# Kernel tuning notes

Hardware: AMD Instinct MI355X
Metric: run time of the kernel (lower is better)

## Reference

```python
import jax, jax.numpy as jnp
import numpy as np

E = 4      # num_ensemble
DIN = 256  # input_dim
D = 256    # d_model (output_dim)
B = 16
T = 1024
LN_EPS = 1e-5


def setup_inputs() -> dict:
    key = jax.random.key(0)
    ks = jax.random.split(key, 14)
    s = 0.02
    x = jax.random.normal(ks[0], (B, T, DIN), dtype=jnp.float32)
    in_proj_w = s * jax.random.normal(ks[1], (3, E, DIN, D), dtype=jnp.float32)
    in_proj_b = jnp.zeros((3, E, D), dtype=jnp.float32)
    mid_w = s * jax.random.normal(ks[2], (2, E, D, D), dtype=jnp.float32)
    mid_b = jnp.zeros((2, E, D), dtype=jnp.float32)
    ff_w1 = s * jax.random.normal(ks[3], (E, D, D), dtype=jnp.float32)
    ff_b1 = jnp.zeros((E, D), dtype=jnp.float32)
    ff_w2 = s * jax.random.normal(ks[4], (E, D, D), dtype=jnp.float32)
    ff_b2 = jnp.zeros((E, D), dtype=jnp.float32)
    ln_w = jnp.ones((E, D), dtype=jnp.float32)
    ln_b = jnp.zeros((E, D), dtype=jnp.float32)
    # LRU initializer (r_min=0.9, r_max=0.999)
    r_min, r_max = 0.9, 0.999
    u1 = jax.random.uniform(ks[5], (E, D), dtype=jnp.float32)
    u2 = jax.random.uniform(ks[6], (E, D), dtype=jnp.float32)
    nu_log = jnp.log(-0.5 * jnp.log(u1 * (r_max ** 2 - r_min ** 2) + r_min ** 2))
    theta_log = jnp.log(u2 * 2.0 * np.pi)
    # |lambda|^2 = exp(-2*exp(nu_log))
    gamma_log = jnp.log(jnp.sqrt(1.0 - jnp.exp(-2.0 * jnp.exp(nu_log))))
    params_log = jnp.stack([nu_log, theta_log, gamma_log], axis=0)  # (3,E,D)
    return {"x": x, "in_proj_w": in_proj_w, "in_proj_b": in_proj_b,
            "params_log": params_log, "mid_w": mid_w, "mid_b": mid_b,
            "ff_w1": ff_w1, "ff_b1": ff_b1, "ff_w2": ff_w2, "ff_b2": ff_b2,
            "ln_w": ln_w, "ln_b": ln_b}


def _forward(x, in_proj_w, in_proj_b, params_log, mid_w, mid_b,
             ff_w1, ff_b1, ff_w2, ff_b2, ln_w, ln_b):
    # in_proj: 3 ensemble linears -> u: (3, E, B, T, D)
    u = jnp.einsum('bti,keio->kebto', x, in_proj_w) + in_proj_b[:, :, None, None, :]
    input_real, input_imag, o = u[0], u[1], u[2]

    params = jnp.exp(params_log)           # (3,E,D)
    nu, theta, gamma = params[0], params[1], params[2]
    mag = jnp.exp(-nu)
    f_real = mag * jnp.cos(theta)          # (E,D)
    f_imag = mag * jnp.sin(theta)

    ir = gamma[:, None, None, :] * input_real  # (E,B,T,D)
    ii = gamma[:, None, None, :] * input_imag

    # complex linear recurrence h_t = f * h_{t-1} + u_t over time axis
    fr = f_real[:, None, :]                # (E,1,D) broadcast over B
    fi = f_imag[:, None, :]
    ir_t = jnp.moveaxis(ir, 2, 0)          # (T,E,B,D)
    ii_t = jnp.moveaxis(ii, 2, 0)

    def step(carry, ut):
        hr, hi = carry
        ur, ui = ut
        hr2 = fr * hr - fi * hi + ur
        hi2 = fr * hi + fi * hr + ui
        return (hr2, hi2), (hr2, hi2)

    h0 = (jnp.zeros((E, B, D), x.dtype), jnp.zeros((E, B, D), x.dtype))
    (hr_last, hi_last), (out_r_t, out_i_t) = jax.lax.scan(step, h0, (ir_t, ii_t))
    output_real = jnp.moveaxis(out_r_t, 0, 2)  # (E,B,T,D)
    output_imag = jnp.moveaxis(out_i_t, 0, 2)

    # hidden packing: (1, B, 2*E*D) with ensemble blocks concatenated, real then imag
    hr_pack = jnp.transpose(hr_last, (1, 0, 2)).reshape(B, E * D)
    hi_pack = jnp.transpose(hi_last, (1, 0, 2)).reshape(B, E * D)
    hidden = jnp.concatenate([hr_pack, hi_pack], axis=-1)[None]  # (1,B,2ED)

    # middle_proj: 2 ensemble linears applied to (real, imag)
    stacked = jnp.stack([output_real, output_imag], axis=0)  # (2,E,B,T,D)
    mid = jnp.einsum('kebtd,kedo->kebto', stacked, mid_w) + mid_b[:, :, None, None, :]
    out = mid[0] - mid[1] + o                                # (E,B,T,D)

    # EnsemblePositionWiseFeedForward (dropout=0 -> identity)
    h1 = jax.nn.gelu(jnp.einsum('ebtd,edo->ebto', out, ff_w1)
                     + ff_b1[:, None, None, :], approximate=False)
    h2 = jnp.einsum('ebtd,edo->ebto', h1, ff_w2) + ff_b2[:, None, None, :] + out
    # LayerNorm over joint (E, D) dims for each (b, t)
    mean = jnp.mean(h2, axis=(0, 3), keepdims=True)
    var = jnp.var(h2, axis=(0, 3), keepdims=True)
    out_ln = (h2 - mean) / jnp.sqrt(var + LN_EPS)
    out_ln = out_ln * ln_w[:, None, None, :] + ln_b[:, None, None, :]
    return out_ln, hidden


def reference(x, in_proj_w, in_proj_b, params_log, mid_w, mid_b,
              ff_w1, ff_b1, ff_w2, ff_b2, ln_w, ln_b):
    return _forward(x, in_proj_w, in_proj_b, params_log, mid_w, mid_b,
                    ff_w1, ff_b1, ff_w2, ff_b2, ln_w, ln_b)
```

## Files before the change

kernel.cpp:

```cpp
#include <hip/hip_runtime.h>
#include <stdint.h>

#define BT_ 16384
#define TT  1024
#define CHUNKS 32
#define CLEN   32
#define LANES  16384

typedef __bf16 bf16x8 __attribute__((ext_vector_type(8)));
typedef float  f32x4  __attribute__((ext_vector_type(4)));
typedef unsigned int u32x4 __attribute__((ext_vector_type(4)));
typedef unsigned short u16;

__device__ __forceinline__ float b2f(u16 s){
    union { float f; unsigned int u; } c; c.u = ((unsigned int)s) << 16; return c.f;
}
__device__ __forceinline__ u16 f2b(float f){
    union { float f; unsigned int u; } c; c.f = f;
    unsigned int u = c.u;
    return (u16)((u + 0x7fffu + ((u >> 16) & 1u)) >> 16);
}

__device__ __forceinline__ void gload_lds16(const u16* g, u16* lds){
    __builtin_amdgcn_global_load_lds(
        (const __attribute__((address_space(1))) void*)g,
        (__attribute__((address_space(3))) void*)lds, 16, 0, 0);
}

__global__ __launch_bounds__(256) void conv_k(const float* __restrict__ x, u16* __restrict__ xc)
{
    long i = ((long)blockIdx.x * 256 + threadIdx.x) * 8;
    float4 v0 = *reinterpret_cast<const float4*>(x + i);
    float4 v1 = *reinterpret_cast<const float4*>(x + i + 4);
    union { u16 s[8]; u32x4 v; } p;
    p.s[0] = f2b(v0.x); p.s[1] = f2b(v0.y); p.s[2] = f2b(v0.z); p.s[3] = f2b(v0.w);
    p.s[4] = f2b(v1.x); p.s[5] = f2b(v1.y); p.s[6] = f2b(v1.z); p.s[7] = f2b(v1.w);
    *reinterpret_cast<u32x4*>(xc + i) = p.v;
}

__global__ __launch_bounds__(256) void prep_w(
    const float* __restrict__ ipw, const float* __restrict__ mw,
    const float* __restrict__ fw1, const float* __restrict__ fw2,
    u16* __restrict__ d_ipw, u16* __restrict__ d_mw,
    u16* __restrict__ d_fw1, u16* __restrict__ d_fw2)
{
    __shared__ u16 tile[64][72];
    int blk = blockIdx.x;
    int w = blk >> 4, t = blk & 15;
    int tr = (t >> 2) * 64;
    int tc = (t & 3) * 64;
    const float* src; u16* dst; int ostride; float sign = 1.f;
    if (w < 12)      { src = ipw + (size_t)w * 65536; dst = d_ipw + (size_t)w * 65536; ostride = 256; }
    else if (w < 20) { int u = w - 12, c = u >> 2, e = u & 3;
                       src = mw + (size_t)u * 65536;
                       dst = d_mw + (size_t)e * 131072 + c * 256; ostride = 512;
                       if (c) sign = -1.f; }
    else if (w < 24) { int e = w - 20; src = fw1 + (size_t)e * 65536; dst = d_fw1 + (size_t)e * 65536; ostride = 256; }
    else             { int e = w - 24; src = fw2 + (size_t)e * 65536; dst = d_fw2 + (size_t)e * 65536; ostride = 256; }

    int q = threadIdx.x;
    int r = q >> 2, cb = (q & 3) * 16;
#pragma unroll
    for (int j = 0; j < 4; j++) {
        int col = cb + j * 4;
        const float4 v = *reinterpret_cast<const float4*>(src + (size_t)(tr + r) * 256 + tc + col);
        tile[r][col + 0] = f2b(v.x * sign);
        tile[r][col + 1] = f2b(v.y * sign);
        tile[r][col + 2] = f2b(v.z * sign);
        tile[r][col + 3] = f2b(v.w * sign);
    }
    __syncthreads();
    int ol = q >> 2, ib = (q & 3) * 16;
    union { u16 s[8]; u32x4 v; } p0, p1;
#pragma unroll
    for (int k = 0; k < 8; k++) { p0.s[k] = tile[ib + k][ol]; p1.s[k] = tile[ib + 8 + k][ol]; }
    u16* drow = dst + (size_t)(tc + ol) * ostride + tr + ib;
    *reinterpret_cast<u32x4*>(drow)     = p0.v;
    *reinterpret_cast<u32x4*>(drow + 8) = p1.v;
}

__global__ __launch_bounds__(256, 3) void gemm_k(
    const u16* __restrict__ A0, const u16* __restrict__ B0,
    const float* __restrict__ biasf, const u16* __restrict__ aux,
    const float* __restrict__ gamlogf, u16* __restrict__ out0,
    u16* __restrict__ out1, int K, int mode)
{
    __shared__ __align__(16) u16 As [128 * 64];
    __shared__ __align__(16) u16 Bs2[128 * 64];
    __shared__ __align__(16) float fs_all[4][512];

    int tid  = threadIdx.x;
    int wave = tid >> 6, lane = tid & 63;
    int quad = lane >> 4, l16 = lane & 15;
    int wm = wave >> 1, wn = wave & 1;
    int m0 = blockIdx.x * 128, n0 = blockIdx.y * 128;
    int z = blockIdx.z;
    int e, k3 = 0;
    const u16* A;
    const u16* Bm;
    if (mode == 1) { k3 = z >> 2; e = z & 3; A = A0; }
    else           { e = z; A = A0 + (size_t)e * BT_ * K; }
    Bm = B0 + (size_t)(mode == 1 ? z : e) * 256 * K;

    int srow8 = lane >> 3, sch = lane & 7;
    int swc = sch ^ srow8;
    const u16* ag[4]; const u16* bg[4]; u16* al[4]; u16* bl[4];
#pragma unroll
    for (int i = 0; i < 4; i++) {
        int ra = wave * 32 + i * 8;
        ag[i] = A  + (size_t)(m0 + ra + srow8) * K + swc * 8;
        bg[i] = Bm + (size_t)(n0 + ra + srow8) * K + swc * 8;
        al[i] = As  + ra * 64;
        bl[i] = Bs2 + ra * 64;
    }

    float* fsw = fs_all[wave];
    int rl8 = lane >> 3, ch = lane & 7;

    int colb = n0 + wn * 64 + ch * 8;
    f32x4 bias_lo, bias_hi;
    f32x4 gam_lo = (f32x4){1.f, 1.f, 1.f, 1.f}, gam_hi = gam_lo;
    if (mode == 1) {
        bias_lo = *reinterpret_cast<const f32x4*>(biasf + z * 256 + colb);
        bias_hi = *reinterpret_cast<const f32x4*>(biasf + z * 256 + colb + 4);
        if (k3 < 2) {
            f32x4 gl = *reinterpret_cast<const f32x4*>(gamlogf + 2048 + e * 256 + colb);
            f32x4 gh = *reinterpret_cast<const f32x4*>(gamlogf + 2048 + e * 256 + colb + 4);
#pragma unroll
            for (int r = 0; r < 4; r++) { gam_lo[r] = expf(gl[r]); gam_hi[r] = expf(gh[r]); }
        }
    } else if (mode == 2) {
        f32x4 a0 = *reinterpret_cast<const f32x4*>(biasf + e * 256 + colb);
        f32x4 a1 = *reinterpret_cast<const f32x4*>(biasf + e * 256 + colb + 4);
        f32x4 c0 = *reinterpret_cast<const f32x4*>(biasf + 1024 + e * 256 + colb);
        f32x4 c1 = *reinterpret_cast<const f32x4*>(biasf + 1024 + e * 256 + colb + 4);
        bias_lo = a0 - c0; bias_hi = a1 - c1;
    } else {
        bias_lo = *reinterpret_cast<const f32x4*>(biasf + e * 256 + colb);
        bias_hi = *reinterpret_cast<const f32x4*>(biasf + e * 256 + colb + 4);
    }

    f32x4 acc[4][4];
#pragma unroll
    for (int i = 0; i < 4; i++)
#pragma unroll
        for (int j = 0; j < 4; j++) acc[i][j] = (f32x4){0.f, 0.f, 0.f, 0.f};

    int nstep = K >> 6;
    for (int st = 0; st < nstep; ++st) {
        if (st) __syncthreads();
#pragma unroll
        for (int i = 0; i < 4; i++) {
            gload_lds16(ag[i], al[i]);
            gload_lds16(bg[i], bl[i]);
            ag[i] += 64; bg[i] += 64;
        }
        __syncthreads();

#pragma unroll
        for (int kt = 0; kt < 2; kt++) {
            bf16x8 afr[4], bfr[4];
#pragma unroll
            for (int f = 0; f < 4; f++) {
                int phys = (kt * 4 + quad) ^ (l16 & 7);
                int rowa = wm * 64 + f * 16 + l16;
                int rowb = wn * 64 + f * 16 + l16;
                union { u32x4 v; bf16x8 b; } u, w;
                u.v = *reinterpret_cast<const u32x4*>(As  + rowa * 64 + phys * 8);
                w.v = *reinterpret_cast<const u32x4*>(Bs2 + rowb * 64 + phys * 8);
                afr[f] = u.b; bfr[f] = w.b;
            }
#pragma unroll
            for (int i = 0; i < 4; i++)
#pragma unroll
                for (int j = 0; j < 4; j++)
                    acc[i][j] = __builtin_amdgcn_mfma_f32_16x16x32_bf16(bfr[j], afr[i], acc[i][j], 0, 0, 0);
        }
    }

#pragma unroll
    for (int s = 0; s < 4; s++) {
#pragma unroll
        for (int p = 0; p < 2; p++) {
            if ((l16 >> 3) == p) {
#pragma unroll
                for (int nf = 0; nf < 4; nf++) {
                    int phys = (nf * 4 + quad) ^ (l16 & 7);
                    *reinterpret_cast<f32x4*>(fsw + (l16 & 7) * 64 + phys * 4) = acc[s][nf];
                }
            }
            asm volatile("" ::: "memory");
            int pa = (2 * ch) ^ rl8;
            f32x4 lo = *reinterpret_cast<const f32x4*>(fsw + rl8 * 64 + pa * 4);
            f32x4 hi = *reinterpret_cast<const f32x4*>(fsw + rl8 * 64 + (pa ^ 1) * 4);
            asm volatile("" ::: "memory");
            lo += bias_lo; hi += bias_hi;
            if (mode == 1) { lo *= gam_lo; hi *= gam_hi; }
            if (mode == 3) {
#pragma unroll
                for (int r = 0; r < 4; r++) {
                    lo[r] = 0.5f * lo[r] * (1.0f + erff(lo[r] * 0.70710678118654752f));
                    hi[r] = 0.5f * hi[r] * (1.0f + erff(hi[r] * 0.70710678118654752f));
                }
            }
            int grow = m0 + wm * 64 + s * 16 + p * 8 + rl8;
            u16* dstp;
            if (mode == 1) {
                if (k3 < 2) dstp = out0 + (((size_t)(e * BT_ + grow)) * 2 + k3) * 256 + colb;
                else        dstp = out1 + ((size_t)e * BT_ + grow) * 256 + colb;
            } else {
                dstp = out0 + ((size_t)e * BT_ + grow) * 256 + colb;
            }
            if (mode == 2 || mode == 4) {
                const u16* ap = aux + ((size_t)e * BT_ + grow) * 256 + colb;
                u32x4 av = *reinterpret_cast<const u32x4*>(ap);
                lo[0] += b2f((u16)(av[0] & 0xffffu)); lo[1] += b2f((u16)(av[0] >> 16));
                lo[2] += b2f((u16)(av[1] & 0xffffu)); lo[3] += b2f((u16)(av[1] >> 16));
                hi[0] += b2f((u16)(av[2] & 0xffffu)); hi[1] += b2f((u16)(av[2] >> 16));
                hi[2] += b2f((u16)(av[3] & 0xffffu)); hi[3] += b2f((u16)(av[3] >> 16));
            }
            u32x4 pv;
            pv[0] = (unsigned int)f2b(lo[0]) | ((unsigned int)f2b(lo[1]) << 16);
            pv[1] = (unsigned int)f2b(lo[2]) | ((unsigned int)f2b(lo[3]) << 16);
            pv[2] = (unsigned int)f2b(hi[0]) | ((unsigned int)f2b(hi[1]) << 16);
            pv[3] = (unsigned int)f2b(hi[2]) | ((unsigned int)f2b(hi[3]) << 16);
            *reinterpret_cast<u32x4*>(dstp) = pv;
        }
    }
}

__global__ __launch_bounds__(256) void scan_a(const u16* __restrict__ u,
    const float* __restrict__ plog, float2* __restrict__ carry)
{
    int l2 = blockIdx.x * 256 + threadIdx.x;
    int chunk = blockIdx.y;
    int dd = (l2 & 127) * 2, b = (l2 >> 7) & 15, e = l2 >> 11;
    float nu0 = expf(plog[e * 256 + dd]),        nu1 = expf(plog[e * 256 + dd + 1]);
    float th0 = expf(plog[1024 + e * 256 + dd]), th1 = expf(plog[1024 + e * 256 + dd + 1]);
    float m0 = expf(-nu0), m1 = expf(-nu1);
    float fr0 = m0 * cosf(th0), fi0 = m0 * sinf(th0);
    float fr1 = m1 * cosf(th1), fi1 = m1 * sinf(th1);
    size_t base = ((size_t)e * BT_ + b * TT) * 512 + (size_t)chunk * CLEN * 512 + dd;
    float hr0 = 0.f, hi0 = 0.f, hr1 = 0.f, hi1 = 0.f;
    for (int t = 0; t < CLEN; t++) {
        unsigned int wr = *reinterpret_cast<const unsigned int*>(u + base);
        unsigned int wi = *reinterpret_cast<const unsigned int*>(u + base + 256);
        float ur0 = b2f((u16)wr), ur1 = b2f((u16)(wr >> 16));
        float ui0 = b2f((u16)wi), ui1 = b2f((u16)(wi >> 16));
        float a0 = fr0 * hr0 - fi0 * hi0 + ur0;
        float b0 = fr0 * hi0 + fi0 * hr0 + ui0;
        float a1 = fr1 * hr1 - fi1 * hi1 + ur1;
        float b1 = fr1 * hi1 + fi1 * hr1 + ui1;
        hr0 = a0; hi0 = b0; hr1 = a1; hi1 = b1;
        base += 512;
    }
    size_t ci = (size_t)chunk * LANES + (size_t)e * 4096 + b * 256 + dd;
    *reinterpret_cast<float4*>(&carry[ci]) = make_float4(hr0, hi0, hr1, hi1);
}

__global__ __launch_bounds__(256) void scan_b(const float* __restrict__ plog,
                                              float2* __restrict__ carry)
{
    int l = blockIdx.x * 256 + threadIdx.x;
    int d = l & 255, e = l >> 12;
    float nu = expf(plog[e * 256 + d]);
    float th = expf(plog[1024 + e * 256 + d]);
    float magL = expf(-nu * (float)CLEN);
    float ang = th * (float)CLEN;
    float frL = magL * cosf(ang), fiL = magL * sinf(ang);
    float gr = 0.f, gi = 0.f;
    for (int j = 0; j < CHUNKS; j++) {
        float2 c = carry[(size_t)j * LANES + l];
        carry[(size_t)j * LANES + l] = make_float2(gr, gi);
        float gr2 = frL * gr - fiL * gi + c.x;
        float gi2 = frL * gi + fiL * gr + c.y;
        gr = gr2; gi = gi2;
    }
}

__global__ __launch_bounds__(256) void scan_c(u16* __restrict__ u,
    const float* __restrict__ plog, const float2* __restrict__ carry,
    float* __restrict__ outh)
{
    int l2 = blockIdx.x * 256 + threadIdx.x;
    int chunk = blockIdx.y;
    int dd = (l2 & 127) * 2, b = (l2 >> 7) & 15, e = l2 >> 11;
    float nu0 = expf(plog[e * 256 + dd]),        nu1 = expf(plog[e * 256 + dd + 1]);
    float th0 = expf(plog[1024 + e * 256 + dd]), th1 = expf(plog[1024 + e * 256 + dd + 1]);
    float m0 = expf(-nu0), m1 = expf(-nu1);
    float fr0 = m0 * cosf(th0), fi0 = m0 * sinf(th0);
    float fr1 = m1 * cosf(th1), fi1 = m1 * sinf(th1);
    size_t base = ((size_t)e * BT_ + b * TT) * 512 + (size_t)chunk * CLEN * 512 + dd;
    size_t ci = (size_t)chunk * LANES + (size_t)e * 4096 + b * 256 + dd;
    float4 c0 = *reinterpret_cast<const float4*>(&carry[ci]);
    float hr0 = c0.x, hi0 = c0.y, hr1 = c0.z, hi1 = c0.w;
    for (int t = 0; t < CLEN; t++) {
        unsigned int wr = *reinterpret_cast<const unsigned int*>(u + base);
        unsigned int wi = *reinterpret_cast<const unsigned int*>(u + base + 256);
        float ur0 = b2f((u16)wr), ur1 = b2f((u16)(wr >> 16));
        float ui0 = b2f((u16)wi), ui1 = b2f((u16)(wi >> 16));
        float a0 = fr0 * hr0 - fi0 * hi0 + ur0;
        float b0 = fr0 * hi0 + fi0 * hr0 + ui0;
        float a1 = fr1 * hr1 - fi1 * hi1 + ur1;
        float b1 = fr1 * hi1 + fi1 * hr1 + ui1;
        hr0 = a0; hi0 = b0; hr1 = a1; hi1 = b1;
        *reinterpret_cast<unsigned int*>(u + base) =
            (unsigned int)f2b(hr0) | ((unsigned int)f2b(hr1) << 16);
        *reinterpret_cast<unsigned int*>(u + base + 256) =
            (unsigned int)f2b(hi0) | ((unsigned int)f2b(hi1) << 16);
        base += 512;
    }
    if (chunk == CHUNKS - 1) {
        float* oh = outh + (size_t)4 * BT_ * 256;
        *reinterpret_cast<float2*>(&oh[b * 2048 + e * 256 + dd])        = make_float2(hr0, hr1);
        *reinterpret_cast<float2*>(&oh[b * 2048 + 1024 + e * 256 + dd]) = make_float2(hi0, hi1);
    }
}

__global__ __launch_bounds__(256) void ln_k(const u16* __restrict__ h2,
    const float* __restrict__ lnw, const float* __restrict__ lnb,
    float* __restrict__ out)
{
    int r = blockIdx.x;
    int d = threadIdx.x;
    float v[4]; float s1 = 0.f, s2 = 0.f;
#pragma unroll
    for (int e = 0; e < 4; e++) {
        float x = b2f(h2[((size_t)e * BT_ + r) * 256 + d]);
        v[e] = x; s1 += x; s2 += x * x;
    }
#pragma unroll
    for (int off = 32; off; off >>= 1) {
        s1 += __shfl_down(s1, off, 64);
        s2 += __shfl_down(s2, off, 64);
    }
    __shared__ float sm[8];
    int wave = threadIdx.x >> 6, lane = threadIdx.x & 63;
    if (lane == 0) { sm[wave] = s1; sm[4 + wave] = s2; }
    __syncthreads();
    float S1 = sm[0] + sm[1] + sm[2] + sm[3];
    float S2 = sm[4] + sm[5] + sm[6] + sm[7];
    float mean = S1 * (1.0f / 1024.0f);
    float var = S2 * (1.0f / 1024.0f) - mean * mean;
    float rstd = rsqrtf(var + 1e-5f);
#pragma unroll
    for (int e = 0; e < 4; e++) {
        float o = (v[e] - mean) * rstd * lnw[e * 256 + d] + lnb[e * 256 + d];
        out[((size_t)e * BT_ + r) * 256 + d] = o;
    }
}

extern "C" void kernel_launch(void* const* d_in, const int* in_sizes, int n_in,
                              void* d_out, int out_size, void* d_ws, size_t ws_size,
                              hipStream_t stream)
{
    const float* x    = (const float*)d_in[0];
    const float* ipw  = (const float*)d_in[1];
    const float* ipb  = (const float*)d_in[2];
    const float* plog = (const float*)d_in[3];
    const float* mw   = (const float*)d_in[4];
    const float* mb   = (const float*)d_in[5];
    const float* fw1  = (const float*)d_in[6];
    const float* fb1  = (const float*)d_in[7];
    const float* fw2  = (const float*)d_in[8];
    const float* fb2  = (const float*)d_in[9];
    const float* lnw  = (const float*)d_in[10];
    const float* lnb  = (const float*)d_in[11];
    float* out = (float*)d_out;

    u16* W = (u16*)d_ws;
    u16* buf_u    = W;
    u16* buf_out  = W + (size_t)33554432;
    u16* xc       = W + (size_t)33554432;
    float2* carry = (float2*)(W + (size_t)37748736);
    u16* buf_mw_t = W + (size_t)50331648;
    u16* c_ipw_t  = W + (size_t)50855936;
    u16* c_fw1_t  = W + (size_t)51642368;
    u16* c_fw2_t  = W + (size_t)51904512;
    u16* scratch  = (u16*)d_out;

    conv_k<<<2048, 256, 0, stream>>>(x, xc);
    prep_w<<<448, 256, 0, stream>>>(ipw, mw, fw1, fw2, c_ipw_t, buf_mw_t, c_fw1_t, c_fw2_t);
    gemm_k<<<dim3(128, 2, 12), 256, 0, stream>>>(xc, c_ipw_t, ipb, nullptr, plog, buf_u, scratch, 256, 1);
    scan_a<<<dim3(32, CHUNKS), 256, 0, stream>>>(buf_u, plog, carry);
    scan_b<<<64, 256, 0, stream>>>(plog, carry);
    scan_c<<<dim3(32, CHUNKS), 256, 0, stream>>>(buf_u, plog, carry, out);
    gemm_k<<<dim3(128, 2, 4), 256, 0, stream>>>(buf_u, buf_mw_t, mb, scratch, nullptr, buf_out, nullptr, 512, 2);
    gemm_k<<<dim3(128, 2, 4), 256, 0, stream>>>(buf_out, c_fw1_t, fb1, nullptr, nullptr, scratch, nullptr, 256, 3);
    gemm_k<<<dim3(128, 2, 4), 256, 0, stream>>>(scratch, c_fw2_t, fb2, buf_out, nullptr, buf_u, nullptr, 256, 4);
    ln_k<<<16384, 256, 0, stream>>>(buf_u, lnw, lnb, out);
}
```

Baseline: 289.3 us.

## Double-buffer LDS tiles in GEMM to overlap global loads with MFMA

Doubles the shared-memory A/B tile buffers so the next K-step's global-to-LDS loads are issued before computing on the current buffer, with one barrier per iteration instead of two. This is meant to hide global load latency behind MFMA work. The larger LDS footprint forces the launch bound down from 3 to 2 blocks per CU, which reduces occupancy. The loads are asynchronous direct-to-LDS and are only waited on by the end-of-iteration barrier, so correctness depends on that barrier draining the outstanding loads.

```diff
diff --git a/kernel.cpp b/kernel.cpp
--- a/kernel.cpp
+++ b/kernel.cpp
@@ -79,14 +79,14 @@
     *reinterpret_cast<u32x4*>(drow + 8) = p1.v;
 }
 
-__global__ __launch_bounds__(256, 3) void gemm_k(
+__global__ __launch_bounds__(256, 2) void gemm_k(
     const u16* __restrict__ A0, const u16* __restrict__ B0,
     const float* __restrict__ biasf, const u16* __restrict__ aux,
     const float* __restrict__ gamlogf, u16* __restrict__ out0,
     u16* __restrict__ out1, int K, int mode)
 {
-    __shared__ __align__(16) u16 As [128 * 64];
-    __shared__ __align__(16) u16 Bs2[128 * 64];
+    __shared__ __align__(16) u16 As [2 * 128 * 64];
+    __shared__ __align__(16) u16 Bs2[2 * 128 * 64];
     __shared__ __align__(16) float fs_all[4][512];
 
     int tid  = threadIdx.x;
@@ -104,14 +104,13 @@
 
     int srow8 = lane >> 3, sch = lane & 7;
     int swc = sch ^ srow8;
-    const u16* ag[4]; const u16* bg[4]; u16* al[4]; u16* bl[4];
+    const u16* ag[4]; const u16* bg[4]; int rb[4];
 #pragma unroll
     for (int i = 0; i < 4; i++) {
         int ra = wave * 32 + i * 8;
+        rb[i] = ra;
         ag[i] = A  + (size_t)(m0 + ra + srow8) * K + swc * 8;
         bg[i] = Bm + (size_t)(n0 + ra + srow8) * K + swc * 8;
-        al[i] = As  + ra * 64;
-        bl[i] = Bs2 + ra * 64;
     }
 
     float* fsw = fs_all[wave];
@@ -147,15 +146,28 @@
         for (int j = 0; j < 4; j++) acc[i][j] = (f32x4){0.f, 0.f, 0.f, 0.f};
 
     int nstep = K >> 6;
+
+#pragma unroll
+    for (int i = 0; i < 4; i++) {
+        gload_lds16(ag[i], As  + rb[i] * 64);
+        gload_lds16(bg[i], Bs2 + rb[i] * 64);
+        ag[i] += 64; bg[i] += 64;
+    }
+    __syncthreads();
+
     for (int st = 0; st < nstep; ++st) {
-        if (st) __syncthreads();
-#pragma unroll
-        for (int i = 0; i < 4; i++) {
-            gload_lds16(ag[i], al[i]);
-            gload_lds16(bg[i], bl[i]);
-            ag[i] += 64; bg[i] += 64;
+        int cur = st & 1;
+        const u16* Ab = As  + cur * 8192;
+        const u16* Bb = Bs2 + cur * 8192;
+        if (st + 1 < nstep) {
+            int nx = cur ^ 1;
+#pragma unroll
+            for (int i = 0; i < 4; i++) {
+                gload_lds16(ag[i], As  + nx * 8192 + rb[i] * 64);
+                gload_lds16(bg[i], Bs2 + nx * 8192 + rb[i] * 64);
+                ag[i] += 64; bg[i] += 64;
+            }
         }
-        __syncthreads();
 
 #pragma unroll
         for (int kt = 0; kt < 2; kt++) {
@@ -166,8 +178,8 @@
                 int rowa = wm * 64 + f * 16 + l16;
                 int rowb = wn * 64 + f * 16 + l16;
                 union { u32x4 v; bf16x8 b; } u, w;
-                u.v = *reinterpret_cast<const u32x4*>(As  + rowa * 64 + phys * 8);
-                w.v = *reinterpret_cast<const u32x4*>(Bs2 + rowb * 64 + phys * 8);
+                u.v = *reinterpret_cast<const u32x4*>(Ab + rowa * 64 + phys * 8);
+                w.v = *reinterpret_cast<const u32x4*>(Bb + rowb * 64 + phys * 8);
                 afr[f] = u.b; bfr[f] = w.b;
             }
 #pragma unroll
@@ -176,6 +188,7 @@
                 for (int j = 0; j < 4; j++)
                     acc[i][j] = __builtin_amdgcn_mfma_f32_16x16x32_bf16(bfr[j], afr[i], acc[i][j], 0, 0, 0);
         }
+        if (st + 1 < nstep) __syncthreads();
     }
 
 #pragma unroll
```

Result: no change. 289.2 us (-0.0%).
